# Kernel tuning notes

Hardware: AMD Instinct MI355X
Metric: run time of the kernel (lower is better)

## Reference

```python
import jax, jax.numpy as jnp
import numpy as np

B, T, D, HS = 8, 2048, 1024, 64  # batch, seq, num_embd, head_size


def setup_inputs() -> dict:
    key = jax.random.key(0)
    kc, kq, kk, kv = jax.random.split(key, 4)
    return {
        "context": jax.random.normal(kc, (B, T, D), dtype=jnp.float32),
        "Wq": jax.random.normal(kq, (D, HS), dtype=jnp.float32) * (D ** -0.5),
        "Wk": jax.random.normal(kk, (D, HS), dtype=jnp.float32) * (D ** -0.5),
        "Wv": jax.random.normal(kv, (D, HS), dtype=jnp.float32) * (D ** -0.5),
    }


def reference(context, Wq, Wk, Wv):
    # context: [B, T, D]; projections: [B, T, HS]
    q = context @ Wq
    k = context @ Wk
    v = context @ Wv
    scale = k.shape[-1] ** -0.5
    # scores: [B, T, T], causal mask, stable softmax (dropout p=0 -> identity)
    wei = jnp.einsum("btd,bsd->bts", q, k) * scale
    t = wei.shape[-1]
    causal = jnp.tril(jnp.ones((t, t), dtype=bool))
    wei = jnp.where(causal, wei, -jnp.inf)
    wei = jax.nn.softmax(wei, axis=-1)
    return jnp.einsum("bts,bsh->bth", wei, v)
```

## Files before the change

### kernel.cpp

```cpp
#include <hip/hip_runtime.h>
#include <math.h>

#define BB 8
#define TT 2048
#define DD 1024
#define HSZ 64

typedef __bf16 bf16_t;
typedef bf16_t bf16x8 __attribute__((ext_vector_type(8)));
typedef bf16_t bf16x4 __attribute__((ext_vector_type(4)));
typedef float f32x4 __attribute__((ext_vector_type(4)));

#define MFMA16(A, B, C) __builtin_amdgcn_mfma_f32_16x16x32_bf16(A, B, C, 0, 0, 0)


__global__ __launch_bounds__(256) void wt_convert(
    const float* __restrict__ Wq, const float* __restrict__ Wk,
    const float* __restrict__ Wv, bf16_t* __restrict__ Wtf)
{
    int id = blockIdx.x * 256 + threadIdx.x;
    int j = id & 7;
    int lane = (id >> 3) & 63;
    int chunk = (id >> 9) & 31;
    int nt = id >> 14;
    int l16 = lane & 15, quad = lane >> 4;
    int k = chunk * 32 + quad * 8 + j;
    int col = nt * 16 + l16;
    int m = col >> 6, ncol = col & 63;
    const float* W = (m == 0) ? Wq : (m == 1) ? Wk : Wv;
    float scl = (m == 0) ? 0.18033688f : 1.0f;
    Wtf[id] = (bf16_t)(W[k * HSZ + ncol] * scl);
}

__global__ __launch_bounds__(256) void qkv_proj(
    const float* __restrict__ ctx, const bf16_t* __restrict__ Wtf,
    bf16_t* __restrict__ Q, bf16_t* __restrict__ Kf, bf16_t* __restrict__ Vf)
{
    __shared__ __align__(16) char smem_raw[32 * 1032 * 2];
    bf16_t (*As)[1032] = (bf16_t (*)[1032])smem_raw;
    f32x4 (*red)[4][4][64] = (f32x4 (*)[4][4][64])smem_raw;

    const int tid = threadIdx.x;
    const int w = tid >> 6, lane = tid & 63;
    const int quad = lane >> 4, l16 = lane & 15;
    const size_t row0 = (size_t)blockIdx.x * 32;
    const int k0 = w * 256;

    {
        const float4* csrc = (const float4*)(ctx + row0 * DD);
        #pragma unroll
        for (int i = 0; i < 32; ++i) {
            float4 v = csrc[i * 256 + tid];
            bf16x4 bv;
            bv[0] = (bf16_t)v.x; bv[1] = (bf16_t)v.y;
            bv[2] = (bf16_t)v.z; bv[3] = (bf16_t)v.w;
            *(bf16x4*)&As[i][tid * 4] = bv;
        }
    }
    __syncthreads();

    f32x4 acc0[12], acc1[12];
    #pragma unroll
    for (int i = 0; i < 12; ++i) {
        acc0[i] = (f32x4){0.f, 0.f, 0.f, 0.f};
        acc1[i] = (f32x4){0.f, 0.f, 0.f, 0.f};
    }

    const bf16_t* wbase = Wtf + lane * 8;

    #pragma unroll
    for (int kc = 0; kc < 256; kc += 32) {
        const int chunk = (k0 + kc) >> 5;
        bf16x8 af0 = *(const bf16x8*)&As[l16][k0 + kc + quad * 8];
        bf16x8 af1 = *(const bf16x8*)&As[16 + l16][k0 + kc + quad * 8];
        #pragma unroll
        for (int nt = 0; nt < 12; ++nt) {
            bf16x8 bfr = *(const bf16x8*)(wbase + ((size_t)nt * 32 + chunk) * 512);
            acc0[nt] = MFMA16(af0, bfr, acc0[nt]);
            acc1[nt] = MFMA16(af1, bfr, acc1[nt]);
        }
    }
    __syncthreads();

    const int bb   = (int)(row0 >> 11);
    const int tloc = (int)(row0 & 2047);
    const int kt   = tloc >> 6;

    #pragma unroll
    for (int r = 0; r < 3; ++r) {
        if (r) __syncthreads();
        #pragma unroll
        for (int i = 0; i < 4; ++i) {
            red[0][w][i][lane] = acc0[r * 4 + i];
            red[1][w][i][lane] = acc1[r * 4 + i];
        }
        __syncthreads();

        #pragma unroll
        for (int m = 0; m < 2; ++m) {
            f32x4 s = red[m][0][w][lane];
            s += red[m][1][w][lane];
            s += red[m][2][w][lane];
            s += red[m][3][w][lane];

            const int tm = tloc + m * 16;

            if (r == 0) {
                const int col = w * 16 + l16;
                #pragma unroll
                for (int reg = 0; reg < 4; ++reg)
                    Q[(row0 + m * 16 + quad * 4 + reg) * HSZ + col] = (bf16_t)s[reg];
            } else if (r == 1) {
                const int nn = (tm >> 4) & 3;
                const int ks = w >> 1;
                const int quadf = (w & 1) * 2 + (l16 >> 3);
                const int jj = l16 & 7;
                const size_t fb = ((((size_t)bb * 32 + kt) * 4 + nn) * 2 + ks) * 512;
                #pragma unroll
                for (int reg = 0; reg < 4; ++reg)
                    Kf[fb + (quadf * 16 + quad * 4 + reg) * 8 + jj] = (bf16_t)s[reg];
            } else {
                const int t0 = tm + quad * 4;
                const int ks = (t0 >> 5) & 1;
                const int quadf = (t0 >> 3) & 3;
                const int j0 = t0 & 7;
                const size_t fb = ((((size_t)bb * 32 + kt) * 2 + ks) * 4 + w) * 512;
                bf16x4 v;
                #pragma unroll
                for (int reg = 0; reg < 4; ++reg) v[reg] = (bf16_t)s[reg];
                *(bf16x4*)(Vf + fb + (quadf * 16 + l16) * 8 + j0) = v;
            }
        }
    }
}

__device__ __forceinline__ void load_kv(
    const bf16_t* __restrict__ Kf, const bf16_t* __restrict__ Vf,
    size_t bofs, int kt, int lane, bf16x8* kf, bf16x8* vf)
{
    const size_t tb = (bofs + (size_t)kt) * 8 * 512;
    const bf16_t* kbase = Kf + tb + lane * 8;
    const bf16_t* vbase = Vf + tb + lane * 8;
    #pragma unroll
    for (int i = 0; i < 8; ++i) {
        kf[i] = *(const bf16x8*)(kbase + i * 512);
        vf[i] = *(const bf16x8*)(vbase + i * 512);
    }
}

#define WREG 8704

__global__ __launch_bounds__(256, 2) void attn_kernel(
    const bf16_t* __restrict__ Q, const bf16_t* __restrict__ Kf,
    const bf16_t* __restrict__ Vf, float* __restrict__ O)
{
    __shared__ __align__(16) char sm[4 * WREG + 512];

    const int tid = threadIdx.x;
    const int w = tid >> 6, lane = tid & 63;
    const int quad = lane >> 4, l16 = lane & 15;

    bf16_t (*Psw)[72] = (bf16_t (*)[72])(sm + w * WREG);
    float  (*Orw)[68] = (float  (*)[68])(sm + w * WREG);
    float* Lred = (float*)(sm + 4 * WREG);

    const int z = blockIdx.x;
    const int b = z & 7;
    const int s = z >> 3;
    const int js = (s < 32) ? (63 - s) : (s - 32);
    const size_t base = (size_t)b * TT * HSZ;
    const size_t bofs = (size_t)b * 32;
    const int ntile = (js >> 1) + 1;
    const int q0 = js << 5;

    bf16x8 qf0[2], qf1[2];
    #pragma unroll
    for (int g = 0; g < 2; ++g) {
        const bf16_t* qp = Q + base + (size_t)(q0 + g * 16 + l16) * HSZ + quad * 8;
        qf0[g] = *(const bf16x8*)qp;
        qf1[g] = *(const bf16x8*)(qp + 32);
    }

    bf16x8 onesA;
    #pragma unroll
    for (int i = 0; i < 8; ++i) onesA[i] = (bf16_t)1.0f;

    f32x4 o[2][4];
    f32x4 lacc[2];
    #pragma unroll
    for (int g = 0; g < 2; ++g) {
        #pragma unroll
        for (int dt = 0; dt < 4; ++dt) o[g][dt] = (f32x4){0.f, 0.f, 0.f, 0.f};
        lacc[g] = (f32x4){0.f, 0.f, 0.f, 0.f};
    }

    bf16x8 kA[8], kB[8], vA[8], vB[8];

    auto process = [&](int kt, const bf16x8* kf, const bf16x8* vf) {
        const bool last = (kt == ntile - 1);

        #pragma unroll
        for (int g = 0; g < 2; ++g) {
            const int jmg = (2 * js + g) & 3;
            const int nv = last ? jmg + 1 : 4;

            f32x4 sc[4];
            __builtin_amdgcn_s_setprio(1);
            #pragma unroll
            for (int n = 0; n < 4; ++n) {
                if (n < nv) {
                    f32x4 a = (f32x4){0.f, 0.f, 0.f, 0.f};
                    a = MFMA16(kf[2 * n], qf0[g], a);
                    a = MFMA16(kf[2 * n + 1], qf1[g], a);
                    sc[n] = a;
                }
            }
            __builtin_amdgcn_s_setprio(0);

            if (last) {
                #pragma unroll
                for (int n = 0; n < 4; ++n) {
                    if (n < nv) {
                        #pragma unroll
                        for (int reg = 0; reg < 4; ++reg) {
                            bool masked = (n == jmg) && (quad * 4 + reg > l16);
                            float p = __builtin_amdgcn_exp2f(sc[n][reg]);
                            sc[n][reg] = masked ? 0.f : p;
                        }
                    }
                }
            } else {
                #pragma unroll
                for (int n = 0; n < 4; ++n)
                    #pragma unroll
                    for (int reg = 0; reg < 4; ++reg)
                        sc[n][reg] = __builtin_amdgcn_exp2f(sc[n][reg]);
            }

            #pragma unroll
            for (int n = 0; n < 4; ++n) {
                bf16x4 pv;
                #pragma unroll
                for (int reg = 0; reg < 4; ++reg)
                    pv[reg] = (bf16_t)((n < nv) ? sc[n][reg] : 0.f);
                *(bf16x4*)&Psw[g * 16 + l16][n * 16 + quad * 4] = pv;
            }
        }

        #pragma unroll
        for (int g = 0; g < 2; ++g) {
            const int nv = last ? ((2 * js + g) & 3) + 1 : 4;
            const int ksm = (nv > 2) ? 2 : 1;
            bf16x8 pf0 = *(const bf16x8*)&Psw[g * 16 + l16][quad * 8];
            bf16x8 pf1 = *(const bf16x8*)&Psw[g * 16 + l16][32 + quad * 8];
            __builtin_amdgcn_s_setprio(1);
            #pragma unroll
            for (int dt = 0; dt < 4; ++dt) {
                o[g][dt] = MFMA16(vf[dt], pf0, o[g][dt]);
                if (ksm == 2) o[g][dt] = MFMA16(vf[4 + dt], pf1, o[g][dt]);
            }
            lacc[g] = MFMA16(onesA, pf0, lacc[g]);
            if (ksm == 2) lacc[g] = MFMA16(onesA, pf1, lacc[g]);
            __builtin_amdgcn_s_setprio(0);
        }
    };

    if (w < ntile) {
        load_kv(Kf, Vf, bofs, w, lane, kA, vA);
        for (int kt = w; kt < ntile; kt += 8) {
            if (kt + 4 < ntile) load_kv(Kf, Vf, bofs, kt + 4, lane, kB, vB);
            process(kt, kA, vA);
            if (kt + 4 < ntile) {
                if (kt + 8 < ntile) load_kv(Kf, Vf, bofs, kt + 8, lane, kA, vA);
                process(kt + 4, kB, vB);
            }
        }
    }

    #pragma unroll
    for (int g = 0; g < 2; ++g) {
        #pragma unroll
        for (int dt = 0; dt < 4; ++dt)
            *(f32x4*)&Orw[g * 16 + l16][dt * 16 + quad * 4] = o[g][dt];
        if (quad == 0) Lred[w * 32 + g * 16 + l16] = lacc[g][0];
    }
    __syncthreads();

    #pragma unroll
    for (int rep = 0; rep < 2; ++rep) {
        const int idx = rep * 256 + tid;
        const int query = idx >> 4, d4 = idx & 15;
        float l = Lred[0 * 32 + query] + Lred[1 * 32 + query] +
                  Lred[2 * 32 + query] + Lred[3 * 32 + query];
        f32x4 sv = *(const f32x4*)((const float*)(sm + 0 * WREG) + query * 68 + d4 * 4);
        sv += *(const f32x4*)((const float*)(sm + 1 * WREG) + query * 68 + d4 * 4);
        sv += *(const f32x4*)((const float*)(sm + 2 * WREG) + query * 68 + d4 * 4);
        sv += *(const f32x4*)((const float*)(sm + 3 * WREG) + query * 68 + d4 * 4);
        const float linv = 1.f / l;
        float4 outv = make_float4(sv[0] * linv, sv[1] * linv,
                                  sv[2] * linv, sv[3] * linv);
        *(float4*)(O + base + (size_t)(q0 + query) * HSZ + d4 * 4) = outv;
    }
}

extern "C" void kernel_launch(void* const* d_in, const int* in_sizes, int n_in,
                              void* d_out, int out_size, void* d_ws, size_t ws_size,
                              hipStream_t stream) {
    const float* ctx = (const float*)d_in[0];
    const float* Wq  = (const float*)d_in[1];
    const float* Wk  = (const float*)d_in[2];
    const float* Wv  = (const float*)d_in[3];
    float* out = (float*)d_out;

    const size_t NQ = (size_t)BB * TT * HSZ;
    bf16_t* Qw  = (bf16_t*)d_ws;
    bf16_t* Kfw = Qw + NQ;
    bf16_t* Vfw = Kfw + NQ;
    bf16_t* Wtf = Vfw + NQ;

    wt_convert<<<768, 256, 0, stream>>>(Wq, Wk, Wv, Wtf);
    qkv_proj<<<512, 256, 0, stream>>>(ctx, Wtf, Qw, Kfw, Vfw);
    attn_kernel<<<512, 256, 0, stream>>>(Qw, Kfw, Vfw, out);
}
```

Before: 123.4 us.

## Software-pipeline QK^T of next tile with PV of current tile

Splits per-tile processing into three stages: score MFMA, exp plus LDS write, and PV MFMA. They are interleaved so the score MFMAs for tile t+4 run alongside the PV MFMAs for tile t. The K fragments now use a single register buffer, V is double-buffered, and the s_setprio hints are removed. The aim is more overlap between matrix-core work and exp/LDS work. The cost is less prefetch distance for K: a freshly loaded K tile is consumed almost at once, which can expose global-load latency.

```diff
diff --git a/kernel.cpp b/kernel.cpp
--- a/kernel.cpp
+++ b/kernel.cpp
@@ -142,10 +142,11 @@
     const bf16_t* kbase = Kf + tb + lane * 8;
     const bf16_t* vbase = Vf + tb + lane * 8;
     #pragma unroll
-    for (int i = 0; i < 8; ++i) {
+    for (int i = 0; i < 8; ++i)
         kf[i] = *(const bf16x8*)(kbase + i * 512);
+    #pragma unroll
+    for (int i = 0; i < 8; ++i)
         vf[i] = *(const bf16x8*)(vbase + i * 512);
-    }
 }
 
 #define WREG 8704
@@ -194,38 +195,41 @@
         lacc[g] = (f32x4){0.f, 0.f, 0.f, 0.f};
     }
 
-    bf16x8 kA[8], kB[8], vA[8], vB[8];
-
-    auto process = [&](int kt, const bf16x8* kf, const bf16x8* vf) {
-        const bool last = (kt == ntile - 1);
-
+    bf16x8 kf[8], vfA[8], vfB[8];
+    f32x4 scA[2][4], scB[2][4];
+
+    auto smfma = [&](int t, f32x4 (*sc)[4]) {
+        const bool lastt = (t == ntile - 1);
         #pragma unroll
         for (int g = 0; g < 2; ++g) {
-            const int jmg = (2 * js + g) & 3;
-            const int nv = last ? jmg + 1 : 4;
-
-            f32x4 sc[4];
-            __builtin_amdgcn_s_setprio(1);
+            const int nv = lastt ? ((2 * js + g) & 3) + 1 : 4;
             #pragma unroll
             for (int n = 0; n < 4; ++n) {
                 if (n < nv) {
                     f32x4 a = (f32x4){0.f, 0.f, 0.f, 0.f};
                     a = MFMA16(kf[2 * n], qf0[g], a);
                     a = MFMA16(kf[2 * n + 1], qf1[g], a);
-                    sc[n] = a;
+                    sc[g][n] = a;
                 }
             }
-            __builtin_amdgcn_s_setprio(0);
-
-            if (last) {
+        }
+    };
+
+    auto expwrite = [&](int t, f32x4 (*sc)[4]) {
+        const bool lastt = (t == ntile - 1);
+        #pragma unroll
+        for (int g = 0; g < 2; ++g) {
+            const int jmg = (2 * js + g) & 3;
+            const int nv = lastt ? jmg + 1 : 4;
+            if (lastt) {
                 #pragma unroll
                 for (int n = 0; n < 4; ++n) {
                     if (n < nv) {
                         #pragma unroll
                         for (int reg = 0; reg < 4; ++reg) {
                             bool masked = (n == jmg) && (quad * 4 + reg > l16);
-                            float p = __builtin_amdgcn_exp2f(sc[n][reg]);
-                            sc[n][reg] = masked ? 0.f : p;
+                            float p = __builtin_amdgcn_exp2f(sc[g][n][reg]);
+                            sc[g][n][reg] = masked ? 0.f : p;
                         }
                     }
                 }
@@ -234,26 +238,27 @@
                 for (int n = 0; n < 4; ++n)
                     #pragma unroll
                     for (int reg = 0; reg < 4; ++reg)
-                        sc[n][reg] = __builtin_amdgcn_exp2f(sc[n][reg]);
-            }
-
+                        sc[g][n][reg] = __builtin_amdgcn_exp2f(sc[g][n][reg]);
+            }
             #pragma unroll
             for (int n = 0; n < 4; ++n) {
                 bf16x4 pv;
                 #pragma unroll
                 for (int reg = 0; reg < 4; ++reg)
-                    pv[reg] = (bf16_t)((n < nv) ? sc[n][reg] : 0.f);
+                    pv[reg] = (bf16_t)((n < nv) ? sc[g][n][reg] : 0.f);
                 *(bf16x4*)&Psw[g * 16 + l16][n * 16 + quad * 4] = pv;
             }
         }
-
+    };
+
+    auto pv = [&](int t, const bf16x8* vf) {
+        const bool lastt = (t == ntile - 1);
         #pragma unroll
         for (int g = 0; g < 2; ++g) {
-            const int nv = last ? ((2 * js + g) & 3) + 1 : 4;
+            const int nv = lastt ? ((2 * js + g) & 3) + 1 : 4;
             const int ksm = (nv > 2) ? 2 : 1;
             bf16x8 pf0 = *(const bf16x8*)&Psw[g * 16 + l16][quad * 8];
             bf16x8 pf1 = *(const bf16x8*)&Psw[g * 16 + l16][32 + quad * 8];
-            __builtin_amdgcn_s_setprio(1);
             #pragma unroll
             for (int dt = 0; dt < 4; ++dt) {
                 o[g][dt] = MFMA16(vf[dt], pf0, o[g][dt]);
@@ -261,19 +266,38 @@
             }
             lacc[g] = MFMA16(onesA, pf0, lacc[g]);
             if (ksm == 2) lacc[g] = MFMA16(onesA, pf1, lacc[g]);
-            __builtin_amdgcn_s_setprio(0);
         }
     };
 
     if (w < ntile) {
-        load_kv(Kf, Vf, bofs, w, lane, kA, vA);
-        for (int kt = w; kt < ntile; kt += 8) {
-            if (kt + 4 < ntile) load_kv(Kf, Vf, bofs, kt + 4, lane, kB, vB);
-            process(kt, kA, vA);
-            if (kt + 4 < ntile) {
-                if (kt + 8 < ntile) load_kv(Kf, Vf, bofs, kt + 8, lane, kA, vA);
-                process(kt + 4, kB, vB);
-            }
+        int t = w;
+        load_kv(Kf, Vf, bofs, t, lane, kf, vfA);
+        smfma(t, scA);
+        if (t + 4 < ntile)
+            load_kv(Kf, Vf, bofs, t + 4, lane, kf, vfB);
+        expwrite(t, scA);
+
+        while (t + 8 < ntile) {
+            smfma(t + 4, scB);
+            pv(t, vfA);
+            expwrite(t + 4, scB);
+            load_kv(Kf, Vf, bofs, t + 8, lane, kf, vfA);
+
+            smfma(t + 8, scA);
+            pv(t + 4, vfB);
+            expwrite(t + 8, scA);
+            if (t + 12 < ntile)
+                load_kv(Kf, Vf, bofs, t + 12, lane, kf, vfB);
+            t += 8;
+        }
+
+        if (t + 4 < ntile) {
+            smfma(t + 4, scB);
+            pv(t, vfA);
+            expwrite(t + 4, scB);
+            pv(t + 4, vfB);
+        } else {
+            pv(t, vfA);
         }
     }
 
```

New measurement: 122.3 us. About the same (-0.9%).
